# Kernel tuning notes

Hardware: AMD Instinct MI355X
Metric: run time of the kernel (lower is better)

The kernel has to match this reference:

```python
import jax, jax.numpy as jnp
import numpy as np

K = 3
STRIDE = 1
PAD = 1
DIL = 1


def _conv2d(x, w, b, stride, pad):
    y = jax.lax.conv_general_dilated(
        x, w, (stride, stride), [(pad, pad), (pad, pad)],
        dimension_numbers=('NCHW', 'OIHW', 'NCHW'))
    return y + b[None, :, None, None]


def setup_inputs() -> dict:
    key = jax.random.key(0)
    ks = jax.random.split(key, 6)
    N, Cin, Cout, H, W = 4, 64, 64, 128, 128
    x = jax.random.normal(ks[0], (N, Cin, H, W), jnp.float32)
    w_off = jax.random.normal(ks[1], (2 * K * K, Cin, K, K), jnp.float32) * 0.01
    b_off = jnp.zeros((2 * K * K,), jnp.float32)
    w_mask = jax.random.normal(ks[2], (K * K, Cin, K, K), jnp.float32) * 0.01
    b_mask = jnp.zeros((K * K,), jnp.float32)
    weight = jax.random.normal(ks[3], (Cout, Cin, K, K), jnp.float32) * 0.05
    bias = jax.random.normal(ks[4], (Cout,), jnp.float32)
    return {"x": x, "w_off": w_off, "b_off": b_off,
            "w_mask": w_mask, "b_mask": b_mask,
            "weight": weight, "bias": bias}


def _deform_conv(x, offset, weight, bias):
    # x: [N,C,H,W]; offset: [N,2*K2,Ho,Wo] with channel layout (dy,dx) per kernel pt
    N, C, H, W = x.shape
    K2 = K * K
    Ho, Wo = offset.shape[2], offset.shape[3]
    off_y = offset[:, 0::2]  # [N,K2,Ho,Wo]
    off_x = offset[:, 1::2]
    ki = jnp.arange(K2) // K
    kj = jnp.arange(K2) % K
    base_y = (jnp.arange(Ho) * STRIDE - PAD)[None, :, None] + (ki * DIL)[:, None, None]
    base_x = (jnp.arange(Wo) * STRIDE - PAD)[None, None, :] + (kj * DIL)[:, None, None]
    py = base_y[None].astype(off_y.dtype) + off_y  # [N,K2,Ho,Wo]
    px = base_x[None].astype(off_x.dtype) + off_x
    y0 = jnp.floor(py)
    x0 = jnp.floor(px)
    wy = py - y0
    wx = px - x0
    xf = x.reshape(N, C, H * W)

    def corner(yi, xi):
        valid = (yi >= 0) & (yi <= H - 1) & (xi >= 0) & (xi <= W - 1)
        yc = jnp.clip(yi, 0, H - 1).astype(jnp.int32)
        xc = jnp.clip(xi, 0, W - 1).astype(jnp.int32)
        idx = (yc * W + xc).reshape(N, -1)  # [N, K2*Ho*Wo]
        g = jnp.take_along_axis(xf, idx[:, None, :], axis=2)  # [N,C,K2*Ho*Wo]
        g = g.reshape(N, C, K2, Ho, Wo)
        return g * valid[:, None].astype(x.dtype)

    # bilinear interpolation with zero padding outside the image
    val = ((1 - wy) * (1 - wx))[:, None] * corner(y0, x0) \
        + ((1 - wy) * wx)[:, None] * corner(y0, x0 + 1) \
        + (wy * (1 - wx))[:, None] * corner(y0 + 1, x0) \
        + (wy * wx)[:, None] * corner(y0 + 1, x0 + 1)  # [N,C,K2,Ho,Wo]
    out = jnp.einsum('nckhw,ock->nohw', val,
                     weight.reshape(weight.shape[0], C, K2))
    return out + bias[None, :, None, None]


def reference(x, w_off, b_off, w_mask, b_mask, weight, bias):
    offset = _conv2d(x, w_off, b_off, STRIDE, PAD)              # [N,2*K2,Ho,Wo]
    mask = jax.nn.sigmoid(_conv2d(x, w_mask, b_mask, STRIDE, PAD))  # [N,K2,Ho,Wo]
    # source does mask.repeat(1,2,1,1) then offset*mask, then plain deform_conv2d
    offset = offset * jnp.concatenate([mask, mask], axis=1)
    return _deform_conv(x, offset, weight, bias)
```

## Files before the change

kernel.cpp:

```cpp
#include <hip/hip_runtime.h>
#include <math.h>

#define HD 128
#define WD 128
#define WP 130
#define CIN 64
#define COUT 64
#define NB 4
#define K2 9
#define HW (HD*WD)
#define CK 576
#define TP 32
#define TPF 16
#define NKK 18

#define WAM   (4 * NKK * 64 * 8)
#define WAO   (2 * NKK * 64 * 8)
#define XTP   ((size_t)NB * WP * WP * CIN)
#define OFFSZ ((size_t)NB * K2 * HW)
#define WTSZ  ((size_t)CK * COUT)

#define PRE_T 1024
#define PRE_H 65
#define PRE_P ((WAM + WAO) / 256)
#define HALO_PER_N 33024
#define HALO_W8 16512

typedef __attribute__((ext_vector_type(8))) short short8;
typedef __attribute__((ext_vector_type(4))) float f32x4;

__device__ inline unsigned short f2bf(float v) {
    unsigned int u = __float_as_uint(v);
    unsigned int r = u + 0x7fffu + ((u >> 16) & 1u);
    return (unsigned short)(r >> 16);
}
__device__ inline float bf2f(unsigned short b) {
    return __uint_as_float(((unsigned int)b) << 16);
}
__device__ inline unsigned int pack_bf16(float a, float b) {
#if __has_builtin(__builtin_amdgcn_cvt_pk_bf16_f32)
    auto r = __builtin_amdgcn_cvt_pk_bf16_f32(a, b);
    unsigned int u; __builtin_memcpy(&u, &r, 4); return u;
#else
    return ((unsigned int)f2bf(b) << 16) | (unsigned int)f2bf(a);
#endif
}
__device__ inline float2 up2(unsigned int u) {
    float2 r;
    r.x = __uint_as_float(u << 16);
    r.y = __uint_as_float(u & 0xffff0000u);
    return r;
}

__global__ __launch_bounds__(256) void pre_kernel(
    const float* __restrict__ x,
    const float* __restrict__ weight,
    const float* __restrict__ w_off,
    const float* __restrict__ w_mask,
    unsigned short* __restrict__ xp,
    short* __restrict__ mhi, short* __restrict__ ohi)
{
    __shared__ float tile[64][66];
    int bid = blockIdx.x;
    int t = threadIdx.x;

    if (bid < PRE_T) {
        int half = bid & 1;
        int h = (bid >> 1) & 127;
        int n = bid >> 8;
        int w0 = half * 64;
        int g = t >> 6, wl = t & 63;
        const float* xb = x + ((size_t)n * CIN) * HW + h * WD + w0;
        #pragma unroll
        for (int i = 0; i < 16; i++) {
            int cc = i * 4 + g;
            tile[wl][cc] = xb[(size_t)cc * HW + wl];
        }
        __syncthreads();
        size_t rowbase = (((size_t)n * WP + (h + 1)) * WP + (w0 + 1)) * CIN;
        #pragma unroll
        for (int i = 0; i < 8; i++) {
            int u = i * 256 + t;
            int ww = u >> 5;
            int cp = (u & 31) * 2;
            float2 v = *(const float2*)&tile[ww][cp];
            *(unsigned int*)&xp[rowbase + (size_t)ww * CIN + cp] = pack_bf16(v.x, v.y);
        }
    } else if (bid < PRE_T + PRE_H) {
        int widx = (bid - PRE_T) * 256 + t;
        if (widx < HALO_W8) {
            int s = widx * 8;
            int n = s / HALO_PER_N;
            int v = s - n * HALO_PER_N;
            size_t nb = (size_t)n * WP * WP * CIN;
            size_t base;
            if (v < 8320) {
                base = nb + v;
            } else if (v < 16640) {
                base = nb + (size_t)129 * WP * CIN + (v - 8320);
            } else if (v < 24832) {
                int v2 = v - 16640; int h = 1 + (v2 >> 6); int c = v2 & 63;
                base = nb + (size_t)h * WP * CIN + c;
            } else {
                int v3 = v - 24832; int h = 1 + (v3 >> 6); int c = v3 & 63;
                base = nb + ((size_t)h * WP + 129) * CIN + c;
            }
            short8 z = {0, 0, 0, 0, 0, 0, 0, 0};
            *(short8*)&xp[base] = z;
        }
    } else {
        int gid = (bid - PRE_T - PRE_H) * 256 + t;
        if (gid < WAM) {
            int idx = gid;
            int jj = idx & 7;
            int lane = (idx >> 3) & 63;
            int kk = (idx >> 9) % NKK;
            int mt = (idx >> 9) / NKK;
            int o = mt * 16 + (lane & 15);
            int rp = kk * 32 + (lane >> 4) * 8 + jj;
            int k = rp >> 6, c = rp & 63;
            mhi[idx] = (short)f2bf(weight[((size_t)o * CIN + c) * 9 + k]);
        } else {
            int idx = gid - WAM;
            int jj = idx & 7;
            int lane = (idx >> 3) & 63;
            int kk = (idx >> 9) % NKK;
            int mt = (idx >> 9) / NKK;
            int j = mt * 16 + (lane & 15);
            int rp = kk * 32 + (lane >> 4) * 8 + jj;
            int k = rp >> 6, c = rp & 63;
            float w = 0.f;
            if (j < 18)      w = w_off[((size_t)j * CIN + c) * 9 + k];
            else if (j < 27) w = w_mask[((size_t)(j - 18) * CIN + c) * 9 + k];
            ohi[idx] = (short)f2bf(w);
        }
    }
}

__global__ __launch_bounds__(256, 3) void fused_kernel(
    const unsigned short* __restrict__ xp,
    const short* __restrict__ waM_hi,
    const short* __restrict__ waO_hi,
    const float* __restrict__ b_off, const float* __restrict__ b_mask,
    const float* __restrict__ bias,
    float* __restrict__ out)
{
    __shared__ __align__(16) short val_hi[72 * 256];
    __shared__ float conv_s[27 * 32];
    __shared__ float4 p_w4[K2 * TP];
    __shared__ int4   p_idx4[K2 * TP];

    int t = threadIdx.x;
    int wv = t >> 6;
    int lane = t & 63;
    int wo0 = blockIdx.x * TP;
    int ho  = blockIdx.y;
    int n   = blockIdx.z;
    const unsigned short* xpn = xp + (size_t)n * WP * WP * CIN;
    int p16 = lane & 15, quad = lane >> 4;

    #pragma unroll
    for (int i = 0; i < 9; i++) {
        int u = t + 256 * i;
        int tap = u >> 8;
        int p = (u >> 3) & 31;
        int g = u & 7;
        int ti = tap / 3, tj = tap - ti * 3;
        const short8 v = *(const short8*)&xpn[((size_t)(ho + ti) * WP + (wo0 + p + tj)) * CIN + g * 8];
        int c2 = tap * 8 + g;
        *(short8*)&val_hi[c2 * 256 + ((p + c2) & 31) * 8] = v;
    }
    __syncthreads();

    {
        int jt = wv >> 1, pt = wv & 1;
        f32x4 acc = {0.f, 0.f, 0.f, 0.f};
        #pragma unroll
        for (int kk = 0; kk < NKK; kk++) {
            int abase = ((jt * NKK + kk) * 64 + lane) * 8;
            short8 ah = *(const short8*)&waO_hi[abase];
            int c2 = kk * 4 + quad;
            short8 b = *(const short8*)&val_hi[c2 * 256 + ((pt * 16 + p16 + c2) & 31) * 8];
            acc = __builtin_amdgcn_mfma_f32_16x16x32_bf16(ah, b, acc, 0, 0, 0);
        }
        #pragma unroll
        for (int i = 0; i < 4; i++) {
            int j = jt * 16 + quad * 4 + i;
            if (j < 27) {
                float bv = (j < 18) ? b_off[j] : b_mask[j - 18];
                conv_s[j * 32 + pt * 16 + p16] = acc[i] + bv;
            }
        }
    }
    __syncthreads();

    #pragma unroll
    for (int pass = 0; pass < 2; pass++) {
        int u = t + pass * 256;
        if (u < K2 * TP) {
            int k = u >> 5, p = u & 31;
            float oy_raw = conv_s[(2 * k) * 32 + p];
            float ox_raw = conv_s[(2 * k + 1) * 32 + p];
            float my = 1.f / (1.f + expf(-conv_s[(18 + (2 * k) % 9) * 32 + p]));
            float mx = 1.f / (1.f + expf(-conv_s[(18 + (2 * k + 1) % 9) * 32 + p]));
            float oy = oy_raw * my;
            float ox = ox_raw * mx;
            int ki = k / 3, kj = k - ki * 3;
            int wo = wo0 + p;
            float py = (float)(ho - 1 + ki) + oy;
            float px = (float)(wo - 1 + kj) + ox;
            float y0f = floorf(py), x0f = floorf(px);
            float wy = py - y0f, wx = px - x0f;
            int y0 = (int)y0f, x0 = (int)x0f;
            float wy0 = 1.f - wy, wx0 = 1.f - wx;
            int y0c = min(max(y0, 0), HD - 1);
            int y1c = min(max(y0 + 1, 0), HD - 1);
            int x0c = min(max(x0, 0), WD - 1);
            int x1c = min(max(x0 + 1, 0), WD - 1);
            bool vy0 = (y0 >= 0) && (y0 < HD);
            bool vy1 = (y0 + 1 >= 0) && (y0 + 1 < HD);
            bool vx0 = (x0 >= 0) && (x0 < WD);
            bool vx1 = (x0 + 1 >= 0) && (x0 + 1 < WD);
            float4 w4;
            w4.x = (vy0 && vx0) ? wy0 * wx0 : 0.f;
            w4.y = (vy0 && vx1) ? wy0 * wx  : 0.f;
            w4.z = (vy1 && vx0) ? wy  * wx0 : 0.f;
            w4.w = (vy1 && vx1) ? wy  * wx  : 0.f;
            int4 i4;
            i4.x = ((y0c + 1) * WP + (x0c + 1)) * CIN;
            i4.y = ((y0c + 1) * WP + (x1c + 1)) * CIN;
            i4.z = ((y1c + 1) * WP + (x0c + 1)) * CIN;
            i4.w = ((y1c + 1) * WP + (x1c + 1)) * CIN;
            p_w4[u] = w4;
            p_idx4[u] = i4;
        }
    }
    __syncthreads();

    #pragma unroll
    for (int i = 0; i < 9; i++) {
        int u = t + 256 * i;
        int task = u >> 3;
        int g = u & 7;
        int c0 = g * 8;
        int k = task >> 5, p = task & 31;
        float4 w4 = p_w4[task];
        int4  i4 = p_idx4[task];
        uint4 qa = *(const uint4*)&xpn[i4.x + c0];
        uint4 qb = *(const uint4*)&xpn[i4.y + c0];
        uint4 qc = *(const uint4*)&xpn[i4.z + c0];
        uint4 qd = *(const uint4*)&xpn[i4.w + c0];
        unsigned int qa_[4] = {qa.x, qa.y, qa.z, qa.w};
        unsigned int qb_[4] = {qb.x, qb.y, qb.z, qb.w};
        unsigned int qc_[4] = {qc.x, qc.y, qc.z, qc.w};
        unsigned int qd_[4] = {qd.x, qd.y, qd.z, qd.w};
        unsigned int r_[4];
        #pragma unroll
        for (int d = 0; d < 4; d++) {
            float2 fa = up2(qa_[d]), fb = up2(qb_[d]), fc = up2(qc_[d]), fd = up2(qd_[d]);
            float2 gg;
            gg.x = w4.x * fa.x + w4.y * fb.x + w4.z * fc.x + w4.w * fd.x;
            gg.y = w4.x * fa.y + w4.y * fb.y + w4.z * fc.y + w4.w * fd.y;
            r_[d] = pack_bf16(gg.x, gg.y);
        }
        uint4 r = {r_[0], r_[1], r_[2], r_[3]};
        int c2 = k * 8 + g;
        *(uint4*)&val_hi[c2 * 256 + ((p + c2) & 31) * 8] = r;
    }
    __syncthreads();

    f32x4 a0 = {0.f, 0.f, 0.f, 0.f};
    f32x4 a1 = {0.f, 0.f, 0.f, 0.f};
    #pragma unroll
    for (int kk = 0; kk < NKK; kk++) {
        int abase = ((wv * NKK + kk) * 64 + lane) * 8;
        short8 ah = *(const short8*)&waM_hi[abase];
        int c2 = kk * 4 + quad;
        short8 b0 = *(const short8*)&val_hi[c2 * 256 + ((p16 + c2) & 31) * 8];
        short8 b1 = *(const short8*)&val_hi[c2 * 256 + ((16 + p16 + c2) & 31) * 8];
        a0 = __builtin_amdgcn_mfma_f32_16x16x32_bf16(ah, b0, a0, 0, 0, 0);
        a1 = __builtin_amdgcn_mfma_f32_16x16x32_bf16(ah, b1, a1, 0, 0, 0);
    }

    size_t obase = ((size_t)n * COUT) * HW + (size_t)ho * WD + wo0;
    #pragma unroll
    for (int i = 0; i < 4; i++) {
        int o = wv * 16 + quad * 4 + i;
        float bv = bias[o];
        out[obase + (size_t)o * HW + p16] = a0[i] + bv;
        out[obase + (size_t)o * HW + 16 + p16] = a1[i] + bv;
    }
}

__global__ void transpose_w_kernel(const float* __restrict__ w, float* __restrict__ wt) {
    int i = blockIdx.x * 256 + threadIdx.x;
    int o = i / CK;
    int ck = i - o * CK;
    wt[ck * COUT + o] = w[i];
}

__global__ __launch_bounds__(256) void offmask_kernel(
    const float* __restrict__ x,
    const float* __restrict__ w_off, const float* __restrict__ b_off,
    const float* __restrict__ w_mask, const float* __restrict__ b_mask,
    float* __restrict__ offy, float* __restrict__ offx)
{
    __shared__ float ws[CK][27];
    int t = threadIdx.x;
    for (int i = t; i < CK * 27; i += 256) {
        int j = i % 27;
        int citap = i / 27;
        int ci = citap / 9;
        int tap = citap - ci * 9;
        float v;
        if (j < 18) v = w_off[(j * CIN + ci) * 9 + tap];
        else        v = w_mask[((j - 18) * CIN + ci) * 9 + tap];
        ws[citap][j] = v;
    }
    __syncthreads();

    int pix = blockIdx.x * 256 + t;
    int n  = pix >> 14;
    int ho = (pix >> 7) & 127;
    int wo = pix & 127;

    float acc[27];
    #pragma unroll
    for (int j = 0; j < 18; j++) acc[j] = b_off[j];
    #pragma unroll
    for (int j = 0; j < 9; j++)  acc[18 + j] = b_mask[j];

    int offs[9];
    bool oks[9];
    #pragma unroll
    for (int dy = 0; dy < 3; dy++) {
        int y = ho - 1 + dy;
        #pragma unroll
        for (int dx = 0; dx < 3; dx++) {
            int xx = wo - 1 + dx;
            bool ok = (y >= 0) && (y < HD) && (xx >= 0) && (xx < WD);
            oks[dy * 3 + dx] = ok;
            offs[dy * 3 + dx] = (ok ? y : 0) * WD + (ok ? xx : 0);
        }
    }
    const float* xn = x + (size_t)n * CIN * HW;
    for (int ci = 0; ci < CIN; ci++) {
        const float* xc = xn + (size_t)ci * HW;
        float v[9];
        #pragma unroll
        for (int tap = 0; tap < 9; tap++)
            v[tap] = oks[tap] ? xc[offs[tap]] : 0.f;
        #pragma unroll
        for (int tap = 0; tap < 9; tap++) {
            const float* wrow = ws[ci * 9 + tap];
            float vv = v[tap];
            #pragma unroll
            for (int j = 0; j < 27; j++) acc[j] += wrow[j] * vv;
        }
    }
    float m[9];
    #pragma unroll
    for (int j = 0; j < 9; j++) m[j] = 1.f / (1.f + expf(-acc[18 + j]));
    #pragma unroll
    for (int k = 0; k < 9; k++) {
        int cy = 2 * k, cx = 2 * k + 1;
        float my = m[cy < 9 ? cy : cy - 9];
        float mx = m[cx < 9 ? cx : cx - 9];
        size_t o = (((size_t)n * K2 + k) * HD + ho) * WD + wo;
        offy[o] = acc[cy] * my;
        offx[o] = acc[cx] * mx;
    }
}

__global__ __launch_bounds__(256) void deform_kernel(
    const float* __restrict__ x,
    const float* __restrict__ offy, const float* __restrict__ offx,
    const float* __restrict__ wt,
    const float* __restrict__ bias,
    float* __restrict__ out)
{
    __shared__ __align__(16) float val_s[CK * TPF];
    __shared__ float4 p_w4[K2 * TPF];
    __shared__ int4   p_idx4[K2 * TPF];

    int t = threadIdx.x;
    int wo0 = blockIdx.x * TPF;
    int ho  = blockIdx.y;
    int n   = blockIdx.z;

    if (t < K2 * TPF) {
        int k = t >> 4, p = t & 15;
        int wo = wo0 + p;
        size_t oi = (((size_t)n * K2 + k) * HD + ho) * WD + wo;
        float oy = offy[oi], ox = offx[oi];
        int ki = k / 3, kj = k - ki * 3;
        float py = (float)(ho - 1 + ki) + oy;
        float px = (float)(wo - 1 + kj) + ox;
        float y0f = floorf(py), x0f = floorf(px);
        float wy = py - y0f, wx = px - x0f;
        int y0 = (int)y0f, x0 = (int)x0f;
        float wy0 = 1.f - wy, wx0 = 1.f - wx;
        int y0c = min(max(y0, 0), HD - 1);
        int y1c = min(max(y0 + 1, 0), HD - 1);
        int x0c = min(max(x0, 0), WD - 1);
        int x1c = min(max(x0 + 1, 0), WD - 1);
        bool vy0 = (y0 >= 0) && (y0 < HD);
        bool vy1 = (y0 + 1 >= 0) && (y0 + 1 < HD);
        bool vx0 = (x0 >= 0) && (x0 < WD);
        bool vx1 = (x0 + 1 >= 0) && (x0 + 1 < WD);
        float4 w4;
        w4.x = (vy0 && vx0) ? wy0 * wx0 : 0.f;
        w4.y = (vy0 && vx1) ? wy0 * wx  : 0.f;
        w4.z = (vy1 && vx0) ? wy  * wx0 : 0.f;
        w4.w = (vy1 && vx1) ? wy  * wx  : 0.f;
        int4 i4;
        i4.x = y0c * WD + x0c;
        i4.y = y0c * WD + x1c;
        i4.z = y1c * WD + x0c;
        i4.w = y1c * WD + x1c;
        p_w4[t] = w4;
        p_idx4[t] = i4;
    }
    __syncthreads();

    const float* xn = x + (size_t)n * CIN * HW;
    for (int e = t; e < CK * TPF; e += 256) {
        int row = e >> 4, p = e & 15;
        int cc = row / 9, k = row - cc * 9;
        int task = (k << 4) | p;
        float4 w4 = p_w4[task];
        int4  i4 = p_idx4[task];
        const float* xc = xn + (size_t)cc * HW;
        val_s[e] = w4.x * xc[i4.x] + w4.y * xc[i4.y]
                 + w4.z * xc[i4.z] + w4.w * xc[i4.w];
    }
    __syncthreads();

    int o = t & 63, q = t >> 6;
    float4 acc = {0.f, 0.f, 0.f, 0.f};
    const float4* v4 = (const float4*)val_s;
    const float* wp = wt + o;
    #pragma unroll 4
    for (int r = 0; r < CK; r++) {
        float w = wp[r * COUT];
        float4 vv = v4[r * 4 + q];
        acc.x += w * vv.x; acc.y += w * vv.y;
        acc.z += w * vv.z; acc.w += w * vv.w;
    }
    float b = bias[o];
    acc.x += b; acc.y += b; acc.z += b; acc.w += b;
    __syncthreads();
    float4* o4 = (float4*)val_s;
    o4[o * 4 + q] = acc;
    __syncthreads();
    size_t obase = ((size_t)n * COUT) * HW + (size_t)ho * WD + wo0;
    #pragma unroll
    for (int i = 0; i < 4; i++) {
        int l = t + 256 * i;
        int oo = l >> 4, p = l & 15;
        out[obase + (size_t)oo * HW + p] = val_s[l];
    }
}

extern "C" void kernel_launch(void* const* d_in, const int* in_sizes, int n_in,
                              void* d_out, int out_size, void* d_ws, size_t ws_size,
                              hipStream_t stream) {
    const float* x      = (const float*)d_in[0];
    const float* w_off  = (const float*)d_in[1];
    const float* b_off  = (const float*)d_in[2];
    const float* w_mask = (const float*)d_in[3];
    const float* b_mask = (const float*)d_in[4];
    const float* weight = (const float*)d_in[5];
    const float* bias   = (const float*)d_in[6];
    float* out = (float*)d_out;

    short* base = (short*)d_ws;
    short* waM_hi = base;
    short* waO_hi = waM_hi + WAM;
    unsigned short* xp = (unsigned short*)(waO_hi + WAO);
    size_t need = ((size_t)WAM + WAO + XTP) * sizeof(short);

    if (ws_size >= need) {
        pre_kernel<<<PRE_T + PRE_H + PRE_P, 256, 0, stream>>>(
            x, weight, w_off, w_mask, xp, waM_hi, waO_hi);
        fused_kernel<<<dim3(WD / TP, HD, NB), 256, 0, stream>>>(
            xp, waM_hi, waO_hi, b_off, b_mask, bias, out);
    } else {
        float* offy = (float*)d_ws;
        float* offx = offy + OFFSZ;
        float* wt   = offx + OFFSZ;
        transpose_w_kernel<<<144, 256, 0, stream>>>(weight, wt);
        offmask_kernel<<<256, 256, 0, stream>>>(x, w_off, b_off, w_mask, b_mask, offy, offx);
        deform_kernel<<<dim3(WD / TPF, HD, NB), 256, 0, stream>>>(x, offy, offx, wt, bias, out);
    }
}
```

Before: 111.9 us.

## Pack bilinear params into half weights and bit-flagged index, raise occupancy to 4

Shrinks per-task bilinear parameters from 32 bytes (float4 weights plus int4 indices) to 12 bytes: two half2 weight pairs and one base index with two flag bits for the x/y neighbour step. The params now share the conv_s shared buffer instead of separate arrays, cutting LDS use, and launch bounds go from 3 to 4 blocks per CU to raise occupancy. The trade-offs are an extra barrier, since values are held in registers until conv_s is dead, some bit-unpacking ALU work, reduced precision in the fp16 interpolation weights, and register pressure under the tighter launch bound.

Measured after the change: 112.5 us. No clear change (+0.5%).

```diff
diff --git a/kernel.cpp b/kernel.cpp
--- a/kernel.cpp
+++ b/kernel.cpp
@@ -1,4 +1,5 @@
 #include <hip/hip_runtime.h>
+#include <hip/hip_fp16.h>
 #include <math.h>
 
 #define HD 128
@@ -13,6 +14,7 @@
 #define TP 32
 #define TPF 16
 #define NKK 18
+#define NTASK (K2*TP)
 
 #define WAM   (4 * NKK * 64 * 8)
 #define WAO   (2 * NKK * 64 * 8)
@@ -137,7 +139,7 @@
     }
 }
 
-__global__ __launch_bounds__(256, 3) void fused_kernel(
+__global__ __launch_bounds__(256, 4) void fused_kernel(
     const unsigned short* __restrict__ xp,
     const short* __restrict__ waM_hi,
     const short* __restrict__ waO_hi,
@@ -146,9 +148,7 @@
     float* __restrict__ out)
 {
     __shared__ __align__(16) short val_hi[72 * 256];
-    __shared__ float conv_s[27 * 32];
-    __shared__ float4 p_w4[K2 * TP];
-    __shared__ int4   p_idx4[K2 * TP];
+    __shared__ __align__(16) unsigned int uparam[864];
 
     int t = threadIdx.x;
     int wv = t >> 6;
@@ -158,6 +158,7 @@
     int n   = blockIdx.z;
     const unsigned short* xpn = xp + (size_t)n * WP * WP * CIN;
     int p16 = lane & 15, quad = lane >> 4;
+    float* conv_s = (float*)uparam;
 
     #pragma unroll
     for (int i = 0; i < 9; i++) {
@@ -194,10 +195,11 @@
     }
     __syncthreads();
 
+    unsigned int r_w01[2], r_w23[2], r_idx[2];
     #pragma unroll
     for (int pass = 0; pass < 2; pass++) {
         int u = t + pass * 256;
-        if (u < K2 * TP) {
+        if (u < NTASK) {
             int k = u >> 5, p = u & 31;
             float oy_raw = conv_s[(2 * k) * 32 + p];
             float ox_raw = conv_s[(2 * k + 1) * 32 + p];
@@ -221,18 +223,29 @@
             bool vy1 = (y0 + 1 >= 0) && (y0 + 1 < HD);
             bool vx0 = (x0 >= 0) && (x0 < WD);
             bool vx1 = (x0 + 1 >= 0) && (x0 + 1 < WD);
-            float4 w4;
-            w4.x = (vy0 && vx0) ? wy0 * wx0 : 0.f;
-            w4.y = (vy0 && vx1) ? wy0 * wx  : 0.f;
-            w4.z = (vy1 && vx0) ? wy  * wx0 : 0.f;
-            w4.w = (vy1 && vx1) ? wy  * wx  : 0.f;
-            int4 i4;
-            i4.x = ((y0c + 1) * WP + (x0c + 1)) * CIN;
-            i4.y = ((y0c + 1) * WP + (x1c + 1)) * CIN;
-            i4.z = ((y1c + 1) * WP + (x0c + 1)) * CIN;
-            i4.w = ((y1c + 1) * WP + (x1c + 1)) * CIN;
-            p_w4[u] = w4;
-            p_idx4[u] = i4;
+            float wa = (vy0 && vx0) ? wy0 * wx0 : 0.f;
+            float wb = (vy0 && vx1) ? wy0 * wx  : 0.f;
+            float wc = (vy1 && vx0) ? wy  * wx0 : 0.f;
+            float wd = (vy1 && vx1) ? wy  * wx  : 0.f;
+            __half2 h01 = __floats2half2_rn(wa, wb);
+            __half2 h23 = __floats2half2_rn(wc, wd);
+            __builtin_memcpy(&r_w01[pass], &h01, 4);
+            __builtin_memcpy(&r_w23[pass], &h23, 4);
+            unsigned int base = (unsigned int)(((y0c + 1) * WP + (x0c + 1)) * CIN);
+            if (x1c > x0c) base |= (1u << 30);
+            if (y1c > y0c) base |= (1u << 31);
+            r_idx[pass] = base;
+        }
+    }
+    __syncthreads();
+
+    #pragma unroll
+    for (int pass = 0; pass < 2; pass++) {
+        int u = t + pass * 256;
+        if (u < NTASK) {
+            uparam[2 * u] = r_w01[pass];
+            uparam[2 * u + 1] = r_w23[pass];
+            uparam[2 * NTASK + u] = r_idx[pass];
         }
     }
     __syncthreads();
@@ -244,12 +257,21 @@
         int g = u & 7;
         int c0 = g * 8;
         int k = task >> 5, p = task & 31;
-        float4 w4 = p_w4[task];
-        int4  i4 = p_idx4[task];
-        uint4 qa = *(const uint4*)&xpn[i4.x + c0];
-        uint4 qb = *(const uint4*)&xpn[i4.y + c0];
-        uint4 qc = *(const uint4*)&xpn[i4.z + c0];
-        uint4 qd = *(const uint4*)&xpn[i4.w + c0];
+        unsigned int w01 = uparam[2 * task];
+        unsigned int w23 = uparam[2 * task + 1];
+        unsigned int pk = uparam[2 * NTASK + task];
+        __half2 h01, h23;
+        __builtin_memcpy(&h01, &w01, 4);
+        __builtin_memcpy(&h23, &w23, 4);
+        float wa = __low2float(h01), wb = __high2float(h01);
+        float wc = __low2float(h23), wd = __high2float(h23);
+        int base = (int)(pk & 0x3fffffffu) + c0;
+        int dx = (pk & (1u << 30)) ? CIN : 0;
+        int dyo = (pk & (1u << 31)) ? WP * CIN : 0;
+        uint4 qa = *(const uint4*)&xpn[base];
+        uint4 qb = *(const uint4*)&xpn[base + dx];
+        uint4 qc = *(const uint4*)&xpn[base + dyo];
+        uint4 qd = *(const uint4*)&xpn[base + dyo + dx];
         unsigned int qa_[4] = {qa.x, qa.y, qa.z, qa.w};
         unsigned int qb_[4] = {qb.x, qb.y, qb.z, qb.w};
         unsigned int qc_[4] = {qc.x, qc.y, qc.z, qc.w};
@@ -259,8 +281,8 @@
         for (int d = 0; d < 4; d++) {
             float2 fa = up2(qa_[d]), fb = up2(qb_[d]), fc = up2(qc_[d]), fd = up2(qd_[d]);
             float2 gg;
-            gg.x = w4.x * fa.x + w4.y * fb.x + w4.z * fc.x + w4.w * fd.x;
-            gg.y = w4.x * fa.y + w4.y * fb.y + w4.z * fc.y + w4.w * fd.y;
+            gg.x = wa * fa.x + wb * fb.x + wc * fc.x + wd * fd.x;
+            gg.y = wa * fa.y + wb * fb.y + wc * fc.y + wd * fd.y;
             r_[d] = pack_bf16(gg.x, gg.y);
         }
         uint4 r = {r_[0], r_[1], r_[2], r_[3]};
```
